# Optimization experiments

Measured on AMD Instinct MI355X. Metric: run time of the kernel, lower is better.

## Reference

```python
import jax, jax.numpy as jnp
import numpy as np

B, C, F, H, W = 8, 16, 256, 112, 112   # batch, cells/image, channels, height, width
NB = 3                                  # tgt_shape = (3, 3) adaptive pool bins


def setup_inputs() -> dict:
    key = jax.random.key(0)
    kf, ky, kx, kry, krx, kn = jax.random.split(key, 6)
    feature_maps = jax.random.normal(kf, (B, F, H, W), jnp.float32)
    N = B * C
    # random rectangular cell blobs with bernoulli interior holes + guaranteed core
    cy = jax.random.randint(ky, (N, 1, 1), 20, H - 20)
    cx = jax.random.randint(kx, (N, 1, 1), 20, W - 20)
    ry = jax.random.randint(kry, (N, 1, 1), 5, 18)
    rx = jax.random.randint(krx, (N, 1, 1), 5, 18)
    yy = jnp.arange(H)[None, :, None]
    xx = jnp.arange(W)[None, None, :]
    rect = (jnp.abs(yy - cy) <= ry) & (jnp.abs(xx - cx) <= rx)
    noise = jax.random.bernoulli(kn, 0.8, (N, H, W))
    core = (jnp.abs(yy - cy) <= 2) & (jnp.abs(xx - cx) <= 2)
    cell_masks = rect & (noise | core)            # [N, H, W] bool, each nonempty
    cell_counts = jnp.full((B,), C, jnp.int32)    # fixed cells per image
    return {"feature_maps": feature_maps, "cell_masks": cell_masks,
            "cell_counts": cell_counts}


def _bin_membership(lo, hi, length):
    # adaptive-pool bin i covers [lo + floor(i*sz/NB), lo + ceil((i+1)*sz/NB))
    i = jnp.arange(NB)
    sz = (hi - lo)[..., None]                      # [B, C, 1]
    start = lo[..., None] + (i * sz) // NB         # [B, C, NB]
    end = lo[..., None] + ((i + 1) * sz + NB - 1) // NB
    pos = jnp.arange(length)
    return (pos >= start[..., None]) & (pos < end[..., None])  # [B, C, NB, L]


def reference(feature_maps, cell_masks, cell_counts):
    Bv, Fv, Hv, Wv = feature_maps.shape
    Cv = cell_masks.shape[0] // Bv
    masks = cell_masks.reshape(Bv, Cv, Hv, Wv)
    # tight bbox per cell (first/last True row and column, exclusive end)
    rows = masks.any(-1)                            # [B, C, H]
    cols = masks.any(-2)                            # [B, C, W]
    y0 = jnp.argmax(rows, -1)
    y1 = Hv - jnp.argmax(rows[..., ::-1], -1)
    x0 = jnp.argmax(cols, -1)
    x1 = Wv - jnp.argmax(cols[..., ::-1], -1)
    ymem = _bin_membership(y0, y1, Hv)              # [B, C, NB, H]
    xmem = _bin_membership(x0, x1, Wv)              # [B, C, NB, W]
    neg = jnp.finfo(feature_maps.dtype).min
    feat = feature_maps[:, None]                    # [B, 1, F, H, W]
    m = masks[:, :, None]                           # [B, C, 1, H, W]
    pooled = []
    for i in range(NB):
        ym = ymem[:, :, i][:, :, None, :, None]     # [B, C, 1, H, 1]
        for j in range(NB):
            xm = xmem[:, :, j][:, :, None, None, :]  # [B, C, 1, 1, W]
            inbin = ym & xm
            # inside bin & mask -> feature; inside bin & ~mask -> 0 (zeroed crop);
            # outside bin -> -inf (excluded from max)
            v = jnp.where(inbin & m, feat, jnp.where(inbin, 0.0, neg))
            pooled.append(v.max((-1, -2)))          # [B, C, F]
    out = jnp.stack(pooled, -1)                     # [B, C, F, 9], index = i*NB + j
    # matches torch pooled.view(-1): flatten order f*9 + i*3 + j
    return out.reshape(Bv * Cv, Fv * NB * NB)
```

## Files before the change

### kernel.cpp

```cpp
#include <hip/hip_runtime.h>
#include <float.h>

#define B_  8
#define C_  16
#define N_  (B_*C_)
#define F_  256
#define H_  112
#define W_  112
#define HW_ (H_*W_)
#define NB_ 3

#define FPAR 4
#define WPB  2
#define FPB  (FPAR*WPB)
#define LMS  64


__global__ __launch_bounds__(256) void bbox_kernel(const int4* __restrict__ mask4,
                                                   int* __restrict__ bb) {
    int n = blockIdx.x, t = threadIdx.x;
    const int4* m = mask4 + (size_t)n * (HW_ / 4);
    int ymin = 1 << 20, ymax = -1, xmin = 1 << 20, xmax = -1;
    for (int i = t; i < HW_ / 4; i += 256) {
        int4 v = m[i];
        int y = i / 28;
        int xb = (i - y * 28) * 4;
        if (v.x | v.y | v.z | v.w) { ymin = min(ymin, y); ymax = max(ymax, y); }
        if (v.x) { xmin = min(xmin, xb);     xmax = max(xmax, xb);     }
        if (v.y) { xmin = min(xmin, xb + 1); xmax = max(xmax, xb + 1); }
        if (v.z) { xmin = min(xmin, xb + 2); xmax = max(xmax, xb + 2); }
        if (v.w) { xmin = min(xmin, xb + 3); xmax = max(xmax, xb + 3); }
    }
    #pragma unroll
    for (int off = 32; off; off >>= 1) {
        ymin = min(ymin, __shfl_xor(ymin, off));
        ymax = max(ymax, __shfl_xor(ymax, off));
        xmin = min(xmin, __shfl_xor(xmin, off));
        xmax = max(xmax, __shfl_xor(xmax, off));
    }
    __shared__ int red[4][4];
    int wave = t >> 6;
    if ((t & 63) == 0) {
        red[wave][0] = ymin; red[wave][1] = ymax;
        red[wave][2] = xmin; red[wave][3] = xmax;
    }
    __syncthreads();
    if (t == 0) {
        for (int w = 1; w < 4; ++w) {
            ymin = min(ymin, red[w][0]); ymax = max(ymax, red[w][1]);
            xmin = min(xmin, red[w][2]); xmax = max(xmax, red[w][3]);
        }
        int y0 = ymin, y1 = ymax + 1, x0 = xmin, x1 = xmax + 1;
        int* o = bb + n * 16;
        o[0] = y0; o[1] = y1; o[2] = x0; o[3] = x1;
        int szy = y1 - y0, szx = x1 - x0;
        for (int i = 0; i < NB_; ++i) {
            o[4+i]  = y0 + (i*szy)/NB_;
            o[7+i]  = y0 + ((i+1)*szy + NB_-1)/NB_;
            o[10+i] = x0 + (i*szx)/NB_;
            o[13+i] = x0 + ((i+1)*szx + NB_-1)/NB_;
        }
    }
}

__global__ __launch_bounds__(128) void pool_kernel(
        const float* __restrict__ feat, const int* __restrict__ mask,
        const int* __restrict__ bb, float* __restrict__ out) {
    int n = blockIdx.x;
    int b = n >> 4;
    const int* o = bb + n * 16;
    int y0 = o[0], x0 = o[2];
    int bh = o[1] - y0, bw = o[3] - x0;
    int x0a = x0 & ~3;
    int x1 = x0 + bw;

    __shared__ float lm[37 * LMS];
    {
        const int* mrow = mask + (size_t)n * HW_ + (size_t)y0 * W_ + x0a;
        int tot = bh * (LMS / 4);
        for (int idx = threadIdx.x; idx < tot; idx += 128) {
            int dy = idx >> 4, g = idx & 15;
            int gx = x0a + 4 * g;
            int4 m4 = *(const int4*)(mrow + (size_t)dy * W_ + 4 * g);
            float4 v;
            v.x = (m4.x && gx     >= x0 && gx     < x1) ? 1.f : 0.f;
            v.y = (m4.y && gx + 1 >= x0 && gx + 1 < x1) ? 1.f : 0.f;
            v.z = (m4.z && gx + 2 >= x0 && gx + 2 < x1) ? 1.f : 0.f;
            v.w = (m4.w && gx + 3 >= x0 && gx + 3 < x1) ? 1.f : 0.f;
            *(float4*)(&lm[dy * LMS + 4 * g]) = v;
        }
    }
    __syncthreads();

    int lane = threadIdx.x & 63, wave = threadIdx.x >> 6;
    int xq = lane & 15, rg = lane >> 4;
    int bi = min(rg, 2);
    int wbw = (x0 - x0a) + bw;
    int xq4 = (4 * xq < wbw) ? 4 * xq : 0;
    int f0 = blockIdx.y * FPB + wave * FPAR;
    const float* gp = feat + (size_t)(b * F_ + f0) * HW_ + (size_t)y0 * W_ + x0a + xq4;

    int ysb  = o[4 + bi];
    int yeb1 = o[7 + bi] - 1;
    int Tmax = max(o[7] - o[4], max(o[8] - o[5], o[9] - o[6]));

    float acc[4][FPAR];
    #pragma unroll
    for (int s = 0; s < 4; ++s)
        #pragma unroll
        for (int pp = 0; pp < FPAR; ++pp) acc[s][pp] = -FLT_MAX;

    for (int t = 0; t < Tmax; ++t) {
        int dy = min(ysb + t, yeb1) - y0;
        int off = dy * W_;
        float4 mv = *(const float4*)(lm + dy * LMS + 4 * xq);
        float4 c[FPAR];
        #pragma unroll
        for (int pp = 0; pp < FPAR; ++pp)
            c[pp] = *(const float4*)(gp + (size_t)pp * HW_ + off);
        #pragma unroll
        for (int pp = 0; pp < FPAR; ++pp) {
            acc[0][pp] = fmaxf(acc[0][pp], mv.x * c[pp].x);
            acc[1][pp] = fmaxf(acc[1][pp], mv.y * c[pp].y);
            acc[2][pp] = fmaxf(acc[2][pp], mv.z * c[pp].z);
            acc[3][pp] = fmaxf(acc[3][pp], mv.w * c[pp].w);
        }
    }

    int xg = x0a + 4 * xq;
    float lim[3][4];
    #pragma unroll
    for (int j = 0; j < 3; ++j) {
        int xs = o[10 + j], xe = o[13 + j];
        #pragma unroll
        for (int s = 0; s < 4; ++s) {
            int xx = xg + s;
            lim[j][s] = (xx >= xs && xx < xe) ? FLT_MAX : -FLT_MAX;
        }
    }
    #pragma unroll
    for (int pp = 0; pp < FPAR; ++pp) {
        float part[3];
        #pragma unroll
        for (int j = 0; j < 3; ++j) {
            float r = fminf(acc[0][pp], lim[j][0]);
            r = fmaxf(r, fminf(acc[1][pp], lim[j][1]));
            r = fmaxf(r, fminf(acc[2][pp], lim[j][2]));
            r = fmaxf(r, fminf(acc[3][pp], lim[j][3]));
            part[j] = r;
        }
        #pragma unroll
        for (int off = 1; off <= 8; off <<= 1) {
            #pragma unroll
            for (int j = 0; j < 3; ++j)
                part[j] = fmaxf(part[j], __shfl_xor(part[j], off));
        }
        if (xq == 0 && rg < 3) {
            float* op = out + (size_t)(n * F_ + f0 + pp) * 9 + rg * 3;
            op[0] = part[0]; op[1] = part[1]; op[2] = part[2];
        }
    }
}

extern "C" void kernel_launch(void* const* d_in, const int* in_sizes, int n_in,
                              void* d_out, int out_size, void* d_ws, size_t ws_size,
                              hipStream_t stream) {
    const float* feat = (const float*)d_in[0];
    const int*   mask = (const int*)d_in[1];
    int* bb = (int*)d_ws;

    bbox_kernel<<<N_, 256, 0, stream>>>((const int4*)mask, bb);
    dim3 grid(N_, F_ / FPB);
    pool_kernel<<<grid, 128, 0, stream>>>(feat, mask, bb, (float*)d_out);
}
```

Before: 175.3 us.

## Read mask directly from global in pool loop and double features per wave

Drops the shared-memory staging of the cropped mask, along with its barrier, and loads the int mask row straight from global memory inside the row loop, using a select in place of a multiply. FPAR doubles from 4 to 8, so each wave handles twice as many feature channels and the grid has half as many blocks along the feature axis. This removes per-block prologue work and redundant mask staging, but adds a global mask load per row iteration and raises register pressure from the larger accumulator array. Columns outside the bbox that the old staging zeroed are still excluded by the final x-bin limits, although they may now contribute 0 instead of the old masked value.

```diff
diff --git a/kernel.cpp b/kernel.cpp
--- a/kernel.cpp
+++ b/kernel.cpp
@@ -10,10 +10,9 @@
 #define HW_ (H_*W_)
 #define NB_ 3
 
-#define FPAR 4
+#define FPAR 8
 #define WPB  2
 #define FPB  (FPAR*WPB)
-#define LMS  64
 
 
 __global__ __launch_bounds__(256) void bbox_kernel(const int4* __restrict__ mask4,
@@ -70,35 +69,18 @@
     int b = n >> 4;
     const int* o = bb + n * 16;
     int y0 = o[0], x0 = o[2];
-    int bh = o[1] - y0, bw = o[3] - x0;
+    int bw = o[3] - x0;
     int x0a = x0 & ~3;
-    int x1 = x0 + bw;
-
-    __shared__ float lm[37 * LMS];
-    {
-        const int* mrow = mask + (size_t)n * HW_ + (size_t)y0 * W_ + x0a;
-        int tot = bh * (LMS / 4);
-        for (int idx = threadIdx.x; idx < tot; idx += 128) {
-            int dy = idx >> 4, g = idx & 15;
-            int gx = x0a + 4 * g;
-            int4 m4 = *(const int4*)(mrow + (size_t)dy * W_ + 4 * g);
-            float4 v;
-            v.x = (m4.x && gx     >= x0 && gx     < x1) ? 1.f : 0.f;
-            v.y = (m4.y && gx + 1 >= x0 && gx + 1 < x1) ? 1.f : 0.f;
-            v.z = (m4.z && gx + 2 >= x0 && gx + 2 < x1) ? 1.f : 0.f;
-            v.w = (m4.w && gx + 3 >= x0 && gx + 3 < x1) ? 1.f : 0.f;
-            *(float4*)(&lm[dy * LMS + 4 * g]) = v;
-        }
-    }
-    __syncthreads();
+    int wbw = (x0 - x0a) + bw;
 
     int lane = threadIdx.x & 63, wave = threadIdx.x >> 6;
     int xq = lane & 15, rg = lane >> 4;
     int bi = min(rg, 2);
-    int wbw = (x0 - x0a) + bw;
     int xq4 = (4 * xq < wbw) ? 4 * xq : 0;
     int f0 = blockIdx.y * FPB + wave * FPAR;
-    const float* gp = feat + (size_t)(b * F_ + f0) * HW_ + (size_t)y0 * W_ + x0a + xq4;
+    size_t rowoff = (size_t)y0 * W_ + x0a + xq4;
+    const float* gp = feat + (size_t)(b * F_ + f0) * HW_ + rowoff;
+    const int*   mp = mask + (size_t)n * HW_ + rowoff;
 
     int ysb  = o[4 + bi];
     int yeb1 = o[7 + bi] - 1;
@@ -111,19 +93,18 @@
         for (int pp = 0; pp < FPAR; ++pp) acc[s][pp] = -FLT_MAX;
 
     for (int t = 0; t < Tmax; ++t) {
-        int dy = min(ysb + t, yeb1) - y0;
-        int off = dy * W_;
-        float4 mv = *(const float4*)(lm + dy * LMS + 4 * xq);
+        int off = (min(ysb + t, yeb1) - y0) * W_;
+        int4 m4 = *(const int4*)(mp + off);
         float4 c[FPAR];
         #pragma unroll
         for (int pp = 0; pp < FPAR; ++pp)
             c[pp] = *(const float4*)(gp + (size_t)pp * HW_ + off);
         #pragma unroll
         for (int pp = 0; pp < FPAR; ++pp) {
-            acc[0][pp] = fmaxf(acc[0][pp], mv.x * c[pp].x);
-            acc[1][pp] = fmaxf(acc[1][pp], mv.y * c[pp].y);
-            acc[2][pp] = fmaxf(acc[2][pp], mv.z * c[pp].z);
-            acc[3][pp] = fmaxf(acc[3][pp], mv.w * c[pp].w);
+            acc[0][pp] = fmaxf(acc[0][pp], m4.x ? c[pp].x : 0.f);
+            acc[1][pp] = fmaxf(acc[1][pp], m4.y ? c[pp].y : 0.f);
+            acc[2][pp] = fmaxf(acc[2][pp], m4.z ? c[pp].z : 0.f);
+            acc[3][pp] = fmaxf(acc[3][pp], m4.w ? c[pp].w : 0.f);
         }
     }
 
```

Result: slower. 191.8 us (+9.4%).
